# Kernel optimization log

Measured on AMD Instinct MI355X. Metric: run time of the kernel, lower is better.

## Reference

```python
import jax, jax.numpy as jnp
import numpy as np


def setup_inputs() -> dict:
    key = jax.random.key(0)
    k1, k2, k3, k4 = jax.random.split(key, 4)
    B, T, d_model, d_internal = 4, 2048, 1024, 64
    x = jax.random.normal(k1, (B, T, d_model), dtype=jnp.float32)
    # torch.nn.Linear weights: [out_features, in_features]
    s = 1.0 / np.sqrt(d_model)
    W_Q = jax.random.uniform(k2, (d_internal, d_model), jnp.float32, -s, s)
    W_K = jax.random.uniform(k3, (d_internal, d_model), jnp.float32, -s, s)
    W_V = jax.random.uniform(k4, (d_internal, d_model), jnp.float32, -s, s)
    return {"x": x, "W_Q": W_Q, "W_K": W_K, "W_V": W_V}


def reference(x, W_Q, W_K, W_V):
    B, T, C = x.shape  # C == d_model
    Q = jnp.einsum('btc,dc->btd', x, W_Q)
    K = jnp.einsum('btc,dc->btd', x, W_K)
    # Faithful to source bug: V is computed with W_K, W_V is unused.
    V = jnp.einsum('btc,dc->btd', x, W_K)
    scale = C ** (-0.5)  # source scales by d_model, not d_internal
    attn = jnp.einsum('btd,bsd->bts', Q, K) * scale  # [B,T,T]
    causal = jnp.tril(jnp.ones((T, T), dtype=bool))
    attn = jnp.where(causal[None, :, :], attn, -jnp.inf)
    attn = jax.nn.softmax(attn, axis=-1)
    return jnp.einsum('bts,bsd->btd', attn, V)
```

## Files before the change

### kernel.cpp

```cpp
#include <hip/hip_runtime.h>
#include <hip/hip_bf16.h>
#include <cstdint>
#include <cstddef>

#define BB 4
#define TT 2048
#define DM 1024
#define DH 64
#define NCH 4

typedef __attribute__((ext_vector_type(8))) short short8;
typedef __attribute__((ext_vector_type(4))) float floatx4;

__device__ __forceinline__ unsigned short f2bf(float f) {
    union { float f; unsigned int u; } v; v.f = f;
    unsigned int u = v.u;
    u += 0x7fffu + ((u >> 16) & 1u);
    return (unsigned short)(u >> 16);
}

__device__ __forceinline__ float bf2f(unsigned short h) {
    union { unsigned int u; float f; } v;
    v.u = ((unsigned int)h) << 16;
    return v.f;
}

__device__ __forceinline__ unsigned int cvtpk(float a, float b) {
    unsigned int r;
    asm("v_cvt_pk_bf16_f32 %0, %1, %2" : "=v"(r) : "v"(a), "v"(b));
    return r;
}

__device__ __forceinline__ short8 cvt8(float4 lo, float4 hi) {
    union { unsigned int u[4]; short8 s; } v;
    v.u[0] = cvtpk(lo.x, lo.y);
    v.u[1] = cvtpk(lo.z, lo.w);
    v.u[2] = cvtpk(hi.x, hi.y);
    v.u[3] = cvtpk(hi.z, hi.w);
    return v.s;
}

#define WTHREADS (8 * 32 * 64)

__global__ __launch_bounds__(256) void wtile_kernel(const float* __restrict__ wq,
                                                    const float* __restrict__ wk,
                                                    unsigned short* __restrict__ wbt) {
    const int j  = blockIdx.x * 256 + threadIdx.x;
    const int l  = j & 63;
    const int kc = (j >> 6) & 31;
    const int nt = j >> 11;
    const float* wbase = (nt < 4) ? wq : wk;
    const float* src = wbase + (size_t)((nt & 3) * 16 + (l & 15)) * DM
                             + kc * 32 + (l >> 4) * 8;
    float4 a = *reinterpret_cast<const float4*>(src);
    float4 b = *reinterpret_cast<const float4*>(src + 4);
    *reinterpret_cast<short8*>(wbt + (size_t)j * 8) = cvt8(a, b);
}

__global__ __launch_bounds__(256) void proj_kernel(const float* __restrict__ x,
                                                   const unsigned short* __restrict__ wbt,
                                                   unsigned short* __restrict__ qo,
                                                   unsigned short* __restrict__ ko,
                                                   unsigned short* __restrict__ kt) {
    __shared__ __align__(16) unsigned short sA[2][16 * 64 * 8];

    const int tid  = threadIdx.x;
    const int wave = tid >> 6;
    const int lane = tid & 63;
    const int col  = lane & 15;
    const int quad = lane >> 4;
    const int mt   = blockIdx.x;

    const float* xtile = x + (size_t)mt * 16 * DM;
    const unsigned short* bq = wbt + ((size_t)wave * 32 * 64) * 8;
    const unsigned short* bk = wbt + ((size_t)(4 + wave) * 32 * 64) * 8;

    floatx4 accQ = (floatx4){0.f, 0.f, 0.f, 0.f};
    floatx4 accK = (floatx4){0.f, 0.f, 0.f, 0.f};

#pragma unroll 4
    for (int i = 0; i < 4; ++i) {
        const int e  = tid + i * 256;
        const int kc = e >> 6;
        const int l  = e & 63;
        const float* src = xtile + (size_t)(l & 15) * DM + kc * 32 + (l >> 4) * 8;
        float4 a = *reinterpret_cast<const float4*>(src);
        float4 b = *reinterpret_cast<const float4*>(src + 4);
        *reinterpret_cast<short8*>(sA[0] + (size_t)e * 8) = cvt8(a, b);
    }
    __syncthreads();

    float4 h1a[4], h1b[4];
#pragma unroll 4
    for (int i = 0; i < 4; ++i) {
        const int e  = tid + i * 256;
        const int kc = 16 + (e >> 6);
        const int l  = e & 63;
        const float* src = xtile + (size_t)(l & 15) * DM + kc * 32 + (l >> 4) * 8;
        h1a[i] = *reinterpret_cast<const float4*>(src);
        h1b[i] = *reinterpret_cast<const float4*>(src + 4);
    }

#pragma unroll
    for (int kc = 0; kc < 16; ++kc) {
        short8 a  = *reinterpret_cast<const short8*>(sA[0] + ((size_t)kc * 64 + lane) * 8);
        short8 b0 = *reinterpret_cast<const short8*>(bq + ((size_t)kc * 64 + lane) * 8);
        short8 b1 = *reinterpret_cast<const short8*>(bk + ((size_t)kc * 64 + lane) * 8);
        accQ = __builtin_amdgcn_mfma_f32_16x16x32_bf16(a, b0, accQ, 0, 0, 0);
        accK = __builtin_amdgcn_mfma_f32_16x16x32_bf16(a, b1, accK, 0, 0, 0);
    }

#pragma unroll 4
    for (int i = 0; i < 4; ++i) {
        const int e = tid + i * 256;
        *reinterpret_cast<short8*>(sA[1] + (size_t)e * 8) = cvt8(h1a[i], h1b[i]);
    }
    __syncthreads();

#pragma unroll
    for (int kc = 0; kc < 16; ++kc) {
        short8 a  = *reinterpret_cast<const short8*>(sA[1] + ((size_t)kc * 64 + lane) * 8);
        short8 b0 = *reinterpret_cast<const short8*>(bq + ((size_t)(16 + kc) * 64 + lane) * 8);
        short8 b1 = *reinterpret_cast<const short8*>(bk + ((size_t)(16 + kc) * 64 + lane) * 8);
        accQ = __builtin_amdgcn_mfma_f32_16x16x32_bf16(a, b0, accQ, 0, 0, 0);
        accK = __builtin_amdgcn_mfma_f32_16x16x32_bf16(a, b1, accK, 0, 0, 0);
    }

    const int g = wave * 16 + col;
    unsigned short hk[4];
#pragma unroll
    for (int r = 0; r < 4; ++r) {
        const size_t row = (size_t)(mt * 16 + quad * 4 + r);
        qo[row * DH + g] = f2bf(accQ[r] * 0.04508422f);
        hk[r] = f2bf(accK[r]);
        ko[row * DH + g] = hk[r];
    }

    __syncthreads();
    unsigned short* kts = (unsigned short*)sA;
#pragma unroll
    for (int r = 0; r < 4; ++r)
        kts[g * 16 + quad * 4 + r] = hk[r];
    __syncthreads();
    if (tid < 128) {
        const int d  = tid >> 1;
        const int s8 = (tid & 1) * 8;
        const int b4 = mt >> 7;
        const int s0 = (mt & 127) * 16 + s8;
        short8 v = *reinterpret_cast<const short8*>(kts + d * 16 + s8);
        *reinterpret_cast<short8*>(kt + ((size_t)(b4 * 64 + d)) * TT + s0) = v;
    }
}

__global__ __launch_bounds__(128) void flash1_kernel(const unsigned short* __restrict__ qb,
                                                     const unsigned short* __restrict__ kb,
                                                     const unsigned short* __restrict__ ktb,
                                                     unsigned short* __restrict__ Opb,
                                                     float* __restrict__ ml) {
    const int c  = blockIdx.x & (NCH - 1);
    const int qt = (blockIdx.x >> 2) & 63;
    const int b  = blockIdx.x >> 8;
    if (16 * c > qt) return;

    __shared__ __align__(16) unsigned short Pl[2][8][16][40];

    const int tid  = threadIdx.x;
    const int wave = tid >> 6;
    const int lane = tid & 63;
    const int col  = lane & 15;
    const int quad = lane >> 4;

    const int q0    = qt * 32;
    const int qrow  = q0 + wave * 16;
    const int s_beg = c * 512;
    const int s_end = min(s_beg + 512, q0 + 32);

    const unsigned short* qp  = qb  + ((size_t)b * TT + qrow) * DH;
    const unsigned short* kp  = kb  + (size_t)b * TT * DH;
    const unsigned short* ktp = ktb + (size_t)b * 64 * TT;

    short8 qf0 = *reinterpret_cast<const short8*>(qp + (size_t)col * DH + quad * 8);
    short8 qf1 = *reinterpret_cast<const short8*>(qp + (size_t)col * DH + 32 + quad * 8);

    floatx4 o[4];
#pragma unroll
    for (int t = 0; t < 4; ++t) o[t] = (floatx4){0.f, 0.f, 0.f, 0.f};
    float lrow[4] = {0.f, 0.f, 0.f, 0.f};
    int   myq[4];
#pragma unroll
    for (int r = 0; r < 4; ++r) myq[r] = qrow + quad * 4 + r;

    auto body = [&](int s0, int slot, bool domask) {
        float sv[2][4];
#pragma unroll
        for (int st = 0; st < 2; ++st) {
            const int skey = s0 + 2 * col + st;
            const unsigned short* kr = kp + (size_t)skey * DH + quad * 8;
            short8 kf0 = *reinterpret_cast<const short8*>(kr);
            short8 kf1 = *reinterpret_cast<const short8*>(kr + 32);
            floatx4 z = (floatx4){0.f, 0.f, 0.f, 0.f};
            z = __builtin_amdgcn_mfma_f32_16x16x32_bf16(qf0, kf0, z, 0, 0, 0);
            z = __builtin_amdgcn_mfma_f32_16x16x32_bf16(qf1, kf1, z, 0, 0, 0);
#pragma unroll
            for (int r = 0; r < 4; ++r) {
                float p = __builtin_exp2f(z[r]);
                if (domask) p = (skey <= myq[r]) ? p : 0.f;
                sv[st][r] = p;
                lrow[r] += p;
            }
        }
#pragma unroll
        for (int r = 0; r < 4; ++r) {
            unsigned int* prow = reinterpret_cast<unsigned int*>(&Pl[wave][slot][quad * 4 + r][0]);
            prow[col] = cvtpk(sv[0][r], sv[1][r]);
        }
        short8 pf = *reinterpret_cast<const short8*>(&Pl[wave][slot][col][quad * 8]);

#pragma unroll
        for (int t = 0; t < 4; ++t) {
            short8 vf = *reinterpret_cast<const short8*>(
                ktp + (size_t)(t * 16 + col) * TT + s0 + quad * 8);
            o[t] = __builtin_amdgcn_mfma_f32_16x16x32_bf16(pf, vf, o[t], 0, 0, 0);
        }
    };

    const int nIter = (s_end - s_beg) >> 5;
#pragma unroll 4
    for (int i = 0; i < nIter; ++i) {
        const int s0 = s_beg + 32 * i;
        body(s0, i & 7, s0 == q0);
    }

#pragma unroll
    for (int m = 1; m < 16; m <<= 1)
#pragma unroll
        for (int r = 0; r < 4; ++r)
            lrow[r] += __shfl_xor(lrow[r], m, 64);

    const int slot = ((b << 6) + qt) * NCH + c;
    unsigned short* op = Opb + (size_t)slot * 2048;
#pragma unroll
    for (int t = 0; t < 4; ++t)
#pragma unroll
        for (int r = 0; r < 4; ++r)
            op[(size_t)(wave * 16 + quad * 4 + r) * DH + t * 16 + col] = f2bf(o[t][r]);
    if (col == 0) {
        float* mlp = ml + (size_t)slot * 32;
#pragma unroll
        for (int r = 0; r < 4; ++r)
            mlp[wave * 16 + quad * 4 + r] = lrow[r];
    }
}

__global__ __launch_bounds__(256) void merge_kernel(const unsigned short* __restrict__ Opb,
                                                    const float* __restrict__ ml,
                                                    float* __restrict__ out) {
    const int qt  = blockIdx.x & 63;
    const int b   = blockIdx.x >> 6;
    const int nch = (qt >> 4) + 1;
    const int t   = threadIdx.x;
    const int row = t >> 3;
    const int c8  = (t & 7) * 8;
    const size_t base = (size_t)blockIdx.x * NCH;

    float L = 0.f;
    float a[8];
#pragma unroll
    for (int i = 0; i < 8; ++i) a[i] = 0.f;
#pragma unroll
    for (int c = 0; c < NCH; ++c) {
        if (c >= nch) break;
        L += ml[(base + c) * 32 + row];
        const unsigned short* p = Opb + (base + c) * 2048 + (size_t)row * 64 + c8;
        short8 v = *reinterpret_cast<const short8*>(p);
#pragma unroll
        for (int j = 0; j < 8; ++j)
            a[j] += bf2f((unsigned short)v[j]);
    }
    const float inv = 1.0f / L;
    float* o = out + ((size_t)b * TT + qt * 32 + row) * DH + c8;
    float4 r0 = {a[0] * inv, a[1] * inv, a[2] * inv, a[3] * inv};
    float4 r1 = {a[4] * inv, a[5] * inv, a[6] * inv, a[7] * inv};
    *reinterpret_cast<float4*>(o)     = r0;
    *reinterpret_cast<float4*>(o + 4) = r1;
}

extern "C" void kernel_launch(void* const* d_in, const int* in_sizes, int n_in,
                              void* d_out, int out_size, void* d_ws, size_t ws_size,
                              hipStream_t stream) {
    const float* x  = (const float*)d_in[0];
    const float* wq = (const float*)d_in[1];
    const float* wk = (const float*)d_in[2];

    unsigned short* wbt = (unsigned short*)d_ws;
    unsigned short* qo  = wbt + (size_t)WTHREADS * 8;
    unsigned short* ko  = qo + (size_t)BB * TT * DH;
    unsigned short* kt  = ko + (size_t)BB * TT * DH;
    unsigned short* Opb = kt + (size_t)BB * DH * TT;
    float* ml  = (float*)(Opb + (size_t)(BB * 64 * NCH) * 2048);
    float* out = (float*)d_out;

    hipLaunchKernelGGL(wtile_kernel,  dim3(WTHREADS / 256),   dim3(256), 0, stream, wq, wk, wbt);
    hipLaunchKernelGGL(proj_kernel,   dim3((BB * TT) / 16),   dim3(256), 0, stream, x, wbt, qo, ko, kt);
    hipLaunchKernelGGL(flash1_kernel, dim3(BB * 64 * NCH),    dim3(128), 0, stream, qo, ko, kt, Opb, ml);
    hipLaunchKernelGGL(merge_kernel,  dim3(BB * 64),          dim3(256), 0, stream, Opb, ml, out);
}
```

Before: 123.2 us.

## Fuse split-K flash chunks and merge into one block with LDS reduction

Each query tile is now processed by a single 512-thread block in which pairs of waves handle the key chunks. Partial outputs and row sums are reduced through shared memory, and the block writes the normalized result directly. This removes the separate merge kernel launch and the global round trip of bf16 partial outputs, which also gives the partials fp32 precision. In exchange the grid has fewer blocks. Waves assigned to chunks beyond the causal limit sit idle at the barrier, so early query tiles use only a quarter of their waves.

```diff
diff --git a/kernel.cpp b/kernel.cpp
--- a/kernel.cpp
+++ b/kernel.cpp
@@ -152,137 +152,125 @@
     }
 }
 
-__global__ __launch_bounds__(128) void flash1_kernel(const unsigned short* __restrict__ qb,
-                                                     const unsigned short* __restrict__ kb,
-                                                     const unsigned short* __restrict__ ktb,
-                                                     unsigned short* __restrict__ Opb,
-                                                     float* __restrict__ ml) {
-    const int c  = blockIdx.x & (NCH - 1);
-    const int qt = (blockIdx.x >> 2) & 63;
-    const int b  = blockIdx.x >> 8;
-    if (16 * c > qt) return;
-
-    __shared__ __align__(16) unsigned short Pl[2][8][16][40];
+__global__ __launch_bounds__(512) void flash_kernel(const unsigned short* __restrict__ qb,
+                                                    const unsigned short* __restrict__ kb,
+                                                    const unsigned short* __restrict__ ktb,
+                                                    float* __restrict__ out) {
+    const int qt = blockIdx.x & 63;
+    const int b  = blockIdx.x >> 6;
+
+    __shared__ __align__(16) unsigned short Pl[8][4][16][40];
+    __shared__ __align__(16) float Ored[NCH][32][68];
+    __shared__ float lred[NCH][32];
 
     const int tid  = threadIdx.x;
-    const int wave = tid >> 6;
+    const int wv   = tid >> 6;
+    const int c    = wv >> 1;
+    const int h    = wv & 1;
     const int lane = tid & 63;
     const int col  = lane & 15;
     const int quad = lane >> 4;
 
-    const int q0    = qt * 32;
-    const int qrow  = q0 + wave * 16;
-    const int s_beg = c * 512;
-    const int s_end = min(s_beg + 512, q0 + 32);
-
-    const unsigned short* qp  = qb  + ((size_t)b * TT + qrow) * DH;
-    const unsigned short* kp  = kb  + (size_t)b * TT * DH;
-    const unsigned short* ktp = ktb + (size_t)b * 64 * TT;
-
-    short8 qf0 = *reinterpret_cast<const short8*>(qp + (size_t)col * DH + quad * 8);
-    short8 qf1 = *reinterpret_cast<const short8*>(qp + (size_t)col * DH + 32 + quad * 8);
-
-    floatx4 o[4];
-#pragma unroll
-    for (int t = 0; t < 4; ++t) o[t] = (floatx4){0.f, 0.f, 0.f, 0.f};
-    float lrow[4] = {0.f, 0.f, 0.f, 0.f};
-    int   myq[4];
-#pragma unroll
-    for (int r = 0; r < 4; ++r) myq[r] = qrow + quad * 4 + r;
-
-    auto body = [&](int s0, int slot, bool domask) {
-        float sv[2][4];
-#pragma unroll
-        for (int st = 0; st < 2; ++st) {
-            const int skey = s0 + 2 * col + st;
-            const unsigned short* kr = kp + (size_t)skey * DH + quad * 8;
-            short8 kf0 = *reinterpret_cast<const short8*>(kr);
-            short8 kf1 = *reinterpret_cast<const short8*>(kr + 32);
-            floatx4 z = (floatx4){0.f, 0.f, 0.f, 0.f};
-            z = __builtin_amdgcn_mfma_f32_16x16x32_bf16(qf0, kf0, z, 0, 0, 0);
-            z = __builtin_amdgcn_mfma_f32_16x16x32_bf16(qf1, kf1, z, 0, 0, 0);
+    const int q0   = qt * 32;
+    const int nch  = (qt >> 4) + 1;
+
+    if (c < nch) {
+        const int qrow  = q0 + h * 16;
+        const int s_beg = c * 512;
+        const int s_end = min(s_beg + 512, q0 + 32);
+
+        const unsigned short* qp  = qb  + ((size_t)b * TT + qrow) * DH;
+        const unsigned short* kp  = kb  + (size_t)b * TT * DH;
+        const unsigned short* ktp = ktb + (size_t)b * 64 * TT;
+
+        short8 qf0 = *reinterpret_cast<const short8*>(qp + (size_t)col * DH + quad * 8);
+        short8 qf1 = *reinterpret_cast<const short8*>(qp + (size_t)col * DH + 32 + quad * 8);
+
+        floatx4 o[4];
+#pragma unroll
+        for (int t = 0; t < 4; ++t) o[t] = (floatx4){0.f, 0.f, 0.f, 0.f};
+        float lrow[4] = {0.f, 0.f, 0.f, 0.f};
+        int   myq[4];
+#pragma unroll
+        for (int r = 0; r < 4; ++r) myq[r] = qrow + quad * 4 + r;
+
+        auto body = [&](int s0, int slot, bool domask) {
+            float sv[2][4];
+#pragma unroll
+            for (int st = 0; st < 2; ++st) {
+                const int skey = s0 + 2 * col + st;
+                const unsigned short* kr = kp + (size_t)skey * DH + quad * 8;
+                short8 kf0 = *reinterpret_cast<const short8*>(kr);
+                short8 kf1 = *reinterpret_cast<const short8*>(kr + 32);
+                floatx4 z = (floatx4){0.f, 0.f, 0.f, 0.f};
+                z = __builtin_amdgcn_mfma_f32_16x16x32_bf16(qf0, kf0, z, 0, 0, 0);
+                z = __builtin_amdgcn_mfma_f32_16x16x32_bf16(qf1, kf1, z, 0, 0, 0);
+#pragma unroll
+                for (int r = 0; r < 4; ++r) {
+                    float p = __builtin_exp2f(z[r]);
+                    if (domask) p = (skey <= myq[r]) ? p : 0.f;
+                    sv[st][r] = p;
+                    lrow[r] += p;
+                }
+            }
 #pragma unroll
             for (int r = 0; r < 4; ++r) {
-                float p = __builtin_exp2f(z[r]);
-                if (domask) p = (skey <= myq[r]) ? p : 0.f;
-                sv[st][r] = p;
-                lrow[r] += p;
+                unsigned int* prow = reinterpret_cast<unsigned int*>(&Pl[wv][slot][quad * 4 + r][0]);
+                prow[col] = cvtpk(sv[0][r], sv[1][r]);
             }
+            short8 pf = *reinterpret_cast<const short8*>(&Pl[wv][slot][col][quad * 8]);
+
+#pragma unroll
+            for (int t = 0; t < 4; ++t) {
+                short8 vf = *reinterpret_cast<const short8*>(
+                    ktp + (size_t)(t * 16 + col) * TT + s0 + quad * 8);
+                o[t] = __builtin_amdgcn_mfma_f32_16x16x32_bf16(pf, vf, o[t], 0, 0, 0);
+            }
+        };
+
+        const int nIter = (s_end - s_beg) >> 5;
+#pragma unroll 4
+        for (int i = 0; i < nIter; ++i) {
+            const int s0 = s_beg + 32 * i;
+            body(s0, i & 3, s0 == q0);
         }
-#pragma unroll
-        for (int r = 0; r < 4; ++r) {
-            unsigned int* prow = reinterpret_cast<unsigned int*>(&Pl[wave][slot][quad * 4 + r][0]);
-            prow[col] = cvtpk(sv[0][r], sv[1][r]);
+
+#pragma unroll
+        for (int m = 1; m < 16; m <<= 1)
+#pragma unroll
+            for (int r = 0; r < 4; ++r)
+                lrow[r] += __shfl_xor(lrow[r], m, 64);
+
+#pragma unroll
+        for (int t = 0; t < 4; ++t)
+#pragma unroll
+            for (int r = 0; r < 4; ++r)
+                Ored[c][h * 16 + quad * 4 + r][t * 16 + col] = o[t][r];
+        if (col == 0) {
+#pragma unroll
+            for (int r = 0; r < 4; ++r)
+                lred[c][h * 16 + quad * 4 + r] = lrow[r];
         }
-        short8 pf = *reinterpret_cast<const short8*>(&Pl[wave][slot][col][quad * 8]);
-
-#pragma unroll
-        for (int t = 0; t < 4; ++t) {
-            short8 vf = *reinterpret_cast<const short8*>(
-                ktp + (size_t)(t * 16 + col) * TT + s0 + quad * 8);
-            o[t] = __builtin_amdgcn_mfma_f32_16x16x32_bf16(pf, vf, o[t], 0, 0, 0);
+    }
+    __syncthreads();
+
+    {
+        const int row = tid >> 4;
+        const int c4  = (tid & 15) * 4;
+        float L = 0.f, a0 = 0.f, a1 = 0.f, a2 = 0.f, a3 = 0.f;
+#pragma unroll
+        for (int cc = 0; cc < NCH; ++cc) {
+            if (cc >= nch) break;
+            L  += lred[cc][row];
+            a0 += Ored[cc][row][c4 + 0];
+            a1 += Ored[cc][row][c4 + 1];
+            a2 += Ored[cc][row][c4 + 2];
+            a3 += Ored[cc][row][c4 + 3];
         }
-    };
-
-    const int nIter = (s_end - s_beg) >> 5;
-#pragma unroll 4
-    for (int i = 0; i < nIter; ++i) {
-        const int s0 = s_beg + 32 * i;
-        body(s0, i & 7, s0 == q0);
-    }
-
-#pragma unroll
-    for (int m = 1; m < 16; m <<= 1)
-#pragma unroll
-        for (int r = 0; r < 4; ++r)
-            lrow[r] += __shfl_xor(lrow[r], m, 64);
-
-    const int slot = ((b << 6) + qt) * NCH + c;
-    unsigned short* op = Opb + (size_t)slot * 2048;
-#pragma unroll
-    for (int t = 0; t < 4; ++t)
-#pragma unroll
-        for (int r = 0; r < 4; ++r)
-            op[(size_t)(wave * 16 + quad * 4 + r) * DH + t * 16 + col] = f2bf(o[t][r]);
-    if (col == 0) {
-        float* mlp = ml + (size_t)slot * 32;
-#pragma unroll
-        for (int r = 0; r < 4; ++r)
-            mlp[wave * 16 + quad * 4 + r] = lrow[r];
-    }
-}
-
-__global__ __launch_bounds__(256) void merge_kernel(const unsigned short* __restrict__ Opb,
-                                                    const float* __restrict__ ml,
-                                                    float* __restrict__ out) {
-    const int qt  = blockIdx.x & 63;
-    const int b   = blockIdx.x >> 6;
-    const int nch = (qt >> 4) + 1;
-    const int t   = threadIdx.x;
-    const int row = t >> 3;
-    const int c8  = (t & 7) * 8;
-    const size_t base = (size_t)blockIdx.x * NCH;
-
-    float L = 0.f;
-    float a[8];
-#pragma unroll
-    for (int i = 0; i < 8; ++i) a[i] = 0.f;
-#pragma unroll
-    for (int c = 0; c < NCH; ++c) {
-        if (c >= nch) break;
-        L += ml[(base + c) * 32 + row];
-        const unsigned short* p = Opb + (base + c) * 2048 + (size_t)row * 64 + c8;
-        short8 v = *reinterpret_cast<const short8*>(p);
-#pragma unroll
-        for (int j = 0; j < 8; ++j)
-            a[j] += bf2f((unsigned short)v[j]);
-    }
-    const float inv = 1.0f / L;
-    float* o = out + ((size_t)b * TT + qt * 32 + row) * DH + c8;
-    float4 r0 = {a[0] * inv, a[1] * inv, a[2] * inv, a[3] * inv};
-    float4 r1 = {a[4] * inv, a[5] * inv, a[6] * inv, a[7] * inv};
-    *reinterpret_cast<float4*>(o)     = r0;
-    *reinterpret_cast<float4*>(o + 4) = r1;
+        const float inv = 1.0f / L;
+        float4 r = {a0 * inv, a1 * inv, a2 * inv, a3 * inv};
+        *reinterpret_cast<float4*>(out + ((size_t)b * TT + q0 + row) * DH + c4) = r;
+    }
 }
 
 extern "C" void kernel_launch(void* const* d_in, const int* in_sizes, int n_in,
@@ -296,12 +284,9 @@
     unsigned short* qo  = wbt + (size_t)WTHREADS * 8;
     unsigned short* ko  = qo + (size_t)BB * TT * DH;
     unsigned short* kt  = ko + (size_t)BB * TT * DH;
-    unsigned short* Opb = kt + (size_t)BB * DH * TT;
-    float* ml  = (float*)(Opb + (size_t)(BB * 64 * NCH) * 2048);
     float* out = (float*)d_out;
 
-    hipLaunchKernelGGL(wtile_kernel,  dim3(WTHREADS / 256),   dim3(256), 0, stream, wq, wk, wbt);
-    hipLaunchKernelGGL(proj_kernel,   dim3((BB * TT) / 16),   dim3(256), 0, stream, x, wbt, qo, ko, kt);
-    hipLaunchKernelGGL(flash1_kernel, dim3(BB * 64 * NCH),    dim3(128), 0, stream, qo, ko, kt, Opb, ml);
-    hipLaunchKernelGGL(merge_kernel,  dim3(BB * 64),          dim3(256), 0, stream, Opb, ml, out);
-}
+    hipLaunchKernelGGL(wtile_kernel, dim3(WTHREADS / 256), dim3(256), 0, stream, wq, wk, wbt);
+    hipLaunchKernelGGL(proj_kernel,  dim3((BB * TT) / 16), dim3(256), 0, stream, x, wbt, qo, ko, kt);
+    hipLaunchKernelGGL(flash_kernel, dim3(BB * 64),        dim3(512), 0, stream, qo, ko, kt, out);
+}
```

Result: faster. 117.6 us (-4.5%).
